# Kernel optimization log

Measured on AMD Instinct MI355X. Metric: run time of the kernel, lower is better.

## Reference

```python
import jax, jax.numpy as jnp
import numpy as np

P = 4096        # n_particles
D = 64          # embedding_dim
H = 4           # attention heads
HD = D // H     # head dim
N = 1_000_000   # n_collisions


def setup_inputs() -> dict:
    key = jax.random.key(0)
    ks = jax.random.split(key, 24)
    s = lambda k, shape, fan: jax.random.normal(k, shape, jnp.float32) / np.sqrt(fan)
    inp = {
        'times': jax.random.normal(ks[0], (N,), jnp.float32),
        'momentum_transfers': jax.random.normal(ks[1], (N,), jnp.float32),
        'positions': jax.random.normal(ks[2], (N,), jnp.float32),
        'particle_pairs': jax.random.randint(ks[3], (N, 2), 0, P),
        # event encoder: Linear(3, D)
        'W_enc': s(ks[4], (3, D), 3), 'b_enc': jnp.zeros((D,), jnp.float32),
        # learned particle embeddings
        'pemb': s(ks[5], (P, D), D),
        # MultiheadAttention projections (math layout: y = x @ W + b)
        'Wq': s(ks[6], (D, D), D), 'bq': jnp.zeros((D,), jnp.float32),
        'Wk': s(ks[7], (D, D), D), 'bk': jnp.zeros((D,), jnp.float32),
        'Wv': s(ks[8], (D, D), D), 'bv': jnp.zeros((D,), jnp.float32),
        'Wo': s(ks[9], (D, D), D), 'bo': jnp.zeros((D,), jnp.float32),
        # mass head: Linear(D, D//2) -> ReLU -> Linear(D//2, 1) -> Softplus
        'Wm1': s(ks[10], (D, D // 2), D), 'bm1': jnp.zeros((D // 2,), jnp.float32),
        'Wm2': s(ks[11], (D // 2, 1), D // 2), 'bm2': jnp.zeros((1,), jnp.float32),
        # diameter head
        'Wd1': s(ks[12], (D, D // 2), D), 'bd1': jnp.zeros((D // 2,), jnp.float32),
        'Wd2': s(ks[13], (D // 2, 1), D // 2), 'bd2': jnp.zeros((1,), jnp.float32),
    }
    return inp


def _forward(times, momentum_transfers, positions, particle_pairs,
             W_enc, b_enc, pemb, Wq, bq, Wk, bk, Wv, bv, Wo, bo,
             Wm1, bm1, Wm2, bm2, Wd1, bd1, Wd2, bd2):
    # 1. embed collision events: (N,3) -> (N,D), tanh
    feats = jnp.stack([times, momentum_transfers, positions], axis=-1)
    emb = jnp.tanh(feats @ W_enc + b_enc)  # (N, D)

    # 2. segment-mean pooling into particle bins (both endpoints of each pair)
    idx = particle_pairs.reshape(-1)                     # (2N,)
    vals = jnp.repeat(emb, 2, axis=0)                    # (2N, D) [p1,p2 per event]
    updates = jax.ops.segment_sum(vals, idx, num_segments=P)          # (P, D)
    counts = jax.ops.segment_sum(jnp.ones_like(idx, jnp.float32), idx,
                                 num_segments=P)                      # (P,)
    counts = jnp.clip(counts, 1.0)
    x = pemb + updates / counts[:, None]                 # (P, D)

    # 3. self-attention over particles (batch of 1)
    q = (x @ Wq + bq).reshape(P, H, HD)
    k = (x @ Wk + bk).reshape(P, H, HD)
    v = (x @ Wv + bv).reshape(P, H, HD)
    scale = 1.0 / np.sqrt(HD)
    scores = jnp.einsum('phd,qhd->hpq', q * scale, k)    # (H, P, P)
    attn = jax.nn.softmax(scores, axis=-1)
    ctx = jnp.einsum('hpq,qhd->phd', attn, v).reshape(P, D)
    x = ctx @ Wo + bo                                    # (P, D)

    # 4. prediction heads
    masses = jax.nn.softplus(
        (jax.nn.relu(x @ Wm1 + bm1) @ Wm2 + bm2)).squeeze(-1)  # (P,)
    diameters = jax.nn.softplus(
        (jax.nn.relu(x @ Wd1 + bd1) @ Wd2 + bd2)).squeeze(-1)  # (P,)
    return masses, diameters


def reference(times, momentum_transfers, positions, particle_pairs,
              W_enc, b_enc, pemb, Wq, bq, Wk, bk, Wv, bv, Wo, bo,
              Wm1, bm1, Wm2, bm2, Wd1, bd1, Wd2, bd2):
    return _forward(times, momentum_transfers, positions, particle_pairs,
                    W_enc, b_enc, pemb, Wq, bq, Wk, bk, Wv, bv, Wo, bo,
                    Wm1, bm1, Wm2, bm2, Wd1, bd1, Wd2, bd2)
```

## Files before the change

kernel.cpp:

```cpp
#include <hip/hip_runtime.h>
#include <math.h>

#define NP 1000000
#define NE (2 * NP)
#define P 4096
#define D 64
#define H 4
#define HD 16

#define NB 256
#define PBT 1024

#define KC 8

typedef short s4v __attribute__((ext_vector_type(4)));
typedef short s8v __attribute__((ext_vector_type(8)));
typedef float f4v __attribute__((ext_vector_type(4)));

__device__ __forceinline__ float softplus_f(float x) {
    return fmaxf(x, 0.0f) + log1pf(__expf(-fabsf(x)));
}
__device__ __forceinline__ unsigned short f2bf_rne(float f) {
    unsigned int b = __float_as_uint(f);
    b += 0x7fffu + ((b >> 16) & 1u);
    return (unsigned short)(b >> 16);
}

__global__ void __launch_bounds__(PBT) hist_pass(const int* __restrict__ pairs,
                                                 int* __restrict__ hists) {
    __shared__ int lh[P];
    const int tid = threadIdx.x, blk = blockIdx.x;
    for (int i = tid; i < P; i += PBT) lh[i] = 0;
    __syncthreads();
    const int lo = (int)(((long long)blk * NE) / NB);
    const int hi = (int)(((long long)(blk + 1) * NE) / NB);
    for (int i = lo + tid; i < hi; i += PBT) atomicAdd(&lh[pairs[i]], 1);
    __syncthreads();
    for (int i = tid; i < P; i += PBT) hists[blk * P + i] = lh[i];
}

__global__ void scan_cols(int* __restrict__ hists, int* __restrict__ totals) {
    int bin = blockIdx.x * 128 + threadIdx.x;
    int p = 0;
    for (int blk = 0; blk < NB; ++blk) {
        int t = hists[blk * P + bin];
        hists[blk * P + bin] = p;
        p += t;
    }
    totals[bin] = p;
}

__global__ void __launch_bounds__(1024) scan_bins(const int* __restrict__ totals,
                                                  int* __restrict__ bin_start) {
    __shared__ int sdat[1024];
    const int t = threadIdx.x;
    int a[4]; int s = 0;
#pragma unroll
    for (int k2 = 0; k2 < 4; ++k2) { a[k2] = totals[t * 4 + k2]; s += a[k2]; }
    sdat[t] = s;
    __syncthreads();
    for (int off = 1; off < 1024; off <<= 1) {
        int v = (t >= off) ? sdat[t - off] : 0;
        __syncthreads();
        sdat[t] += v;
        __syncthreads();
    }
    int run = sdat[t] - s;
#pragma unroll
    for (int k2 = 0; k2 < 4; ++k2) { bin_start[t * 4 + k2] = run; run += a[k2]; }
    if (t == 1023) bin_start[P] = run;
}

__global__ void __launch_bounds__(PBT) place_pass(
        const int* __restrict__ pairs, const float* __restrict__ times,
        const float* __restrict__ mom, const float* __restrict__ pos,
        const int* __restrict__ hists, const int* __restrict__ bin_start,
        float4* __restrict__ sfeats) {
    __shared__ int lc[P];
    __shared__ int loff[P];
    const int tid = threadIdx.x, blk = blockIdx.x;
    for (int i = tid; i < P; i += PBT) {
        lc[i] = 0;
        loff[i] = bin_start[i] + hists[blk * P + i];
    }
    __syncthreads();
    const int lo = (int)(((long long)blk * NE) / NB);
    const int hi = (int)(((long long)(blk + 1) * NE) / NB);
    for (int i = lo + tid; i < hi; i += PBT) {
        int b = pairs[i];
        int ev = i >> 1;
        int r = atomicAdd(&lc[b], 1);
        float4 f; f.x = times[ev]; f.y = mom[ev]; f.z = pos[ev]; f.w = 0.0f;
        sfeats[loff[b] + r] = f;
    }
}

#define GBODY(fv)                                                              \
    {                                                                          \
        float u0 = fmaf(fv.x, w0a[0], fmaf(fv.y, w1a[0], fmaf(fv.z, w2a[0], ba[0]))); \
        float u1 = fmaf(fv.x, w0a[1], fmaf(fv.y, w1a[1], fmaf(fv.z, w2a[1], ba[1]))); \
        float u2 = fmaf(fv.x, w0a[2], fmaf(fv.y, w1a[2], fmaf(fv.z, w2a[2], ba[2]))); \
        float u3 = fmaf(fv.x, w0a[3], fmaf(fv.y, w1a[3], fmaf(fv.z, w2a[3], ba[3]))); \
        float u4 = fmaf(fv.x, w0b[0], fmaf(fv.y, w1b[0], fmaf(fv.z, w2b[0], bbv[0]))); \
        float u5 = fmaf(fv.x, w0b[1], fmaf(fv.y, w1b[1], fmaf(fv.z, w2b[1], bbv[1]))); \
        float u6 = fmaf(fv.x, w0b[2], fmaf(fv.y, w1b[2], fmaf(fv.z, w2b[2], bbv[2]))); \
        float u7 = fmaf(fv.x, w0b[3], fmaf(fv.y, w1b[3], fmaf(fv.z, w2b[3], bbv[3]))); \
        racc[0] += __builtin_amdgcn_rcpf(__builtin_amdgcn_exp2f(u0) + 1.0f);   \
        racc[1] += __builtin_amdgcn_rcpf(__builtin_amdgcn_exp2f(u1) + 1.0f);   \
        racc[2] += __builtin_amdgcn_rcpf(__builtin_amdgcn_exp2f(u2) + 1.0f);   \
        racc[3] += __builtin_amdgcn_rcpf(__builtin_amdgcn_exp2f(u3) + 1.0f);   \
        racc[4] += __builtin_amdgcn_rcpf(__builtin_amdgcn_exp2f(u4) + 1.0f);   \
        racc[5] += __builtin_amdgcn_rcpf(__builtin_amdgcn_exp2f(u5) + 1.0f);   \
        racc[6] += __builtin_amdgcn_rcpf(__builtin_amdgcn_exp2f(u6) + 1.0f);   \
        racc[7] += __builtin_amdgcn_rcpf(__builtin_amdgcn_exp2f(u7) + 1.0f);   \
    }

__global__ void __launch_bounds__(512) gather_kernel(
        const float4* __restrict__ sfeats, const int* __restrict__ bin_start,
        const float* __restrict__ Wenc, const float* __restrict__ benc,
        const float* __restrict__ pemb, float* __restrict__ x) {
    __shared__ float sred[4][16][68];
    const int tid = threadIdx.x;
    const int wv = tid >> 6, ln = tid & 63;
    const int bi = wv >> 1, hw = wv & 1;
    const int es = ln & 7, dg = ln >> 3;
    const int b = blockIdx.x * 4 + bi;
    const int d0 = dg * 8;
    const float C = 2.8853900817779268f;
    f4v w0a = *(const f4v*)(Wenc + d0);          f4v w0b = *(const f4v*)(Wenc + d0 + 4);
    f4v w1a = *(const f4v*)(Wenc + D + d0);      f4v w1b = *(const f4v*)(Wenc + D + d0 + 4);
    f4v w2a = *(const f4v*)(Wenc + 2 * D + d0);  f4v w2b = *(const f4v*)(Wenc + 2 * D + d0 + 4);
    f4v ba  = *(const f4v*)(benc + d0);          f4v bbv = *(const f4v*)(benc + d0 + 4);
    w0a *= C; w0b *= C; w1a *= C; w1b *= C; w2a *= C; w2b *= C; ba *= C; bbv *= C;

    const int s0 = bin_start[b], s1 = bin_start[b + 1];
    const int cnt = s1 - s0;
    const int half = (cnt + 1) >> 1;
    const int lo = s0 + hw * half;
    const int hi = hw ? s1 : (s0 + half);

    float racc[8];
#pragma unroll
    for (int j = 0; j < 8; ++j) racc[j] = 0.0f;
    int ncnt = 0;
    int base = lo;
    for (; base + 16 <= hi; base += 16) {
        float4 f0 = sfeats[base + es];
        float4 f1 = sfeats[base + 8 + es];
        GBODY(f0);
        GBODY(f1);
        ncnt += 2;
    }
    if (base + 8 <= hi) {
        float4 f0 = sfeats[base + es];
        GBODY(f0);
        ncnt += 1;
        base += 8;
    }
    if (base < hi) {
        const int n = hi - base;
        const bool valid = es < n;
        float4 f = valid ? sfeats[base + es] : make_float4(0.f, 0.f, 0.f, 0.f);
        float save[8];
#pragma unroll
        for (int j = 0; j < 8; ++j) save[j] = racc[j];
        GBODY(f);
        if (!valid) {
#pragma unroll
            for (int j = 0; j < 8; ++j) racc[j] = save[j];
        } else {
            ncnt += 1;
        }
    }
    const float fn = (float)ncnt;
    float* sw = &sred[bi][hw * 8 + es][d0];
#pragma unroll
    for (int j = 0; j < 8; ++j) sw[j] = fmaf(-2.0f, racc[j], fn);
    __syncthreads();
    if (tid < 256) {
        int bin = tid >> 6, dim = tid & 63;
        float s = 0.0f;
#pragma unroll
        for (int e2 = 0; e2 < 16; ++e2) s += sred[bin][e2][dim];
        int gb = blockIdx.x * 4 + bin;
        float c2 = (float)(bin_start[gb + 1] - bin_start[gb]);
        x[gb * D + dim] = pemb[gb * D + dim] + s / fmaxf(c2, 1.0f);
    }
}

__global__ void qkv_kernel(const float* __restrict__ x,
                           const float* __restrict__ Wq, const float* __restrict__ bq,
                           const float* __restrict__ Wk, const float* __restrict__ bk,
                           const float* __restrict__ Wv, const float* __restrict__ bv,
                           unsigned short* __restrict__ Qb, unsigned short* __restrict__ Kb,
                           unsigned short* __restrict__ Vb) {
    __shared__ float xs[4][D];
    const int r0 = blockIdx.x * 4;
    const int tid = threadIdx.x;
    xs[tid >> 6][tid & 63] = x[r0 * D + tid];
    __syncthreads();
    const int row = tid >> 6, col = tid & 63;
    float aq = bq[col], ak = bk[col], av = bv[col];
    for (int d = 0; d < D; ++d) {
        float xv = xs[row][d];
        aq = fmaf(xv, Wq[d * D + col], aq);
        ak = fmaf(xv, Wk[d * D + col], ak);
        av = fmaf(xv, Wv[d * D + col], av);
    }
    const int h = col >> 4, hd = col & 15, gr = r0 + row;
    Qb[((h * P + gr) << 4) + hd] = f2bf_rne(aq * 0.3606737602222409f);
    Kb[((h * P + gr) << 4) + hd] = f2bf_rne(ak);
    Vb[(size_t)(h * 16 + hd) * P + gr] = f2bf_rne(av);
}

__global__ void __launch_bounds__(256) flash_kernel(
        const unsigned short* __restrict__ Qb, const unsigned short* __restrict__ Kb,
        const unsigned short* __restrict__ Vb,
        float* __restrict__ pl, float* __restrict__ pout) {
    const int bid = blockIdx.x;
    const int h  = bid & 3;
    const int qt = (bid >> 2) & 63;
    const int kc = bid >> 8;
    const int tid = threadIdx.x;
    const int wv = tid >> 6, lane = tid & 63;
    const int g = lane >> 4, li = lane & 15;
    const int q0 = qt * 64 + wv * 16;

    s8v qf = {0, 0, 0, 0, 0, 0, 0, 0};
    {
        s4v ql = *(const s4v*)(Qb + ((size_t)(h * P + q0 + li) << 4) + 4 * g);
        qf[0] = ql[0]; qf[1] = ql[1]; qf[2] = ql[2]; qf[3] = ql[3];
    }
    const unsigned short* Kh = Kb + ((size_t)(h * P) << 4);
    const unsigned short* Vrow = Vb + (size_t)(h * 16 + li) * P;

    f4v accA = {0.f, 0.f, 0.f, 0.f};
    f4v accB = {0.f, 0.f, 0.f, 0.f};
    float lA = 0.f, lB = 0.f;
    const int kbeg = kc * (P / KC);
    const int kend = kbeg + P / KC;
#pragma unroll 2
    for (int k0 = kbeg; k0 < kend; k0 += 64) {
        s4v t1 = *(const s4v*)(Kh + ((size_t)(k0 + li) << 4) + 4 * g);
        s4v t2 = *(const s4v*)(Kh + ((size_t)(k0 + 16 + li) << 4) + 4 * g);
        s4v t3 = *(const s4v*)(Kh + ((size_t)(k0 + 32 + li) << 4) + 4 * g);
        s4v t4 = *(const s4v*)(Kh + ((size_t)(k0 + 48 + li) << 4) + 4 * g);
        s4v v1 = *(const s4v*)(Vrow + k0 + 4 * g);
        s4v v2 = *(const s4v*)(Vrow + k0 + 16 + 4 * g);
        s4v v3 = *(const s4v*)(Vrow + k0 + 32 + 4 * g);
        s4v v4 = *(const s4v*)(Vrow + k0 + 48 + 4 * g);
        s8v ka1 = {t1[0], t1[1], t1[2], t1[3], 0, 0, 0, 0};
        s8v ka2 = {t2[0], t2[1], t2[2], t2[3], 0, 0, 0, 0};
        s8v ka3 = {t3[0], t3[1], t3[2], t3[3], 0, 0, 0, 0};
        s8v ka4 = {t4[0], t4[1], t4[2], t4[3], 0, 0, 0, 0};
        f4v z = {0.f, 0.f, 0.f, 0.f};
        f4v c1 = __builtin_amdgcn_mfma_f32_16x16x32_bf16(ka1, qf, z, 0, 0, 0);
        f4v c2 = __builtin_amdgcn_mfma_f32_16x16x32_bf16(ka2, qf, z, 0, 0, 0);
        f4v c3 = __builtin_amdgcn_mfma_f32_16x16x32_bf16(ka3, qf, z, 0, 0, 0);
        f4v c4 = __builtin_amdgcn_mfma_f32_16x16x32_bf16(ka4, qf, z, 0, 0, 0);
        float p0 = __builtin_amdgcn_exp2f(c1[0]), p1 = __builtin_amdgcn_exp2f(c1[1]);
        float p2 = __builtin_amdgcn_exp2f(c1[2]), p3 = __builtin_amdgcn_exp2f(c1[3]);
        float p4 = __builtin_amdgcn_exp2f(c2[0]), p5 = __builtin_amdgcn_exp2f(c2[1]);
        float p6 = __builtin_amdgcn_exp2f(c2[2]), p7 = __builtin_amdgcn_exp2f(c2[3]);
        float p8 = __builtin_amdgcn_exp2f(c3[0]), p9 = __builtin_amdgcn_exp2f(c3[1]);
        float pa = __builtin_amdgcn_exp2f(c3[2]), pb = __builtin_amdgcn_exp2f(c3[3]);
        float pc = __builtin_amdgcn_exp2f(c4[0]), pd = __builtin_amdgcn_exp2f(c4[1]);
        float pe = __builtin_amdgcn_exp2f(c4[2]), pf_ = __builtin_amdgcn_exp2f(c4[3]);
        lA += ((p0 + p1) + (p2 + p3)) + ((p4 + p5) + (p6 + p7));
        lB += ((p8 + p9) + (pa + pb)) + ((pc + pd) + (pe + pf_));
        s8v pf1, pf2;
        pf1[0] = (short)(__float_as_uint(p0) >> 16); pf1[1] = (short)(__float_as_uint(p1) >> 16);
        pf1[2] = (short)(__float_as_uint(p2) >> 16); pf1[3] = (short)(__float_as_uint(p3) >> 16);
        pf1[4] = (short)(__float_as_uint(p4) >> 16); pf1[5] = (short)(__float_as_uint(p5) >> 16);
        pf1[6] = (short)(__float_as_uint(p6) >> 16); pf1[7] = (short)(__float_as_uint(p7) >> 16);
        pf2[0] = (short)(__float_as_uint(p8) >> 16); pf2[1] = (short)(__float_as_uint(p9) >> 16);
        pf2[2] = (short)(__float_as_uint(pa) >> 16); pf2[3] = (short)(__float_as_uint(pb) >> 16);
        pf2[4] = (short)(__float_as_uint(pc) >> 16); pf2[5] = (short)(__float_as_uint(pd) >> 16);
        pf2[6] = (short)(__float_as_uint(pe) >> 16); pf2[7] = (short)(__float_as_uint(pf_) >> 16);
        s8v vf1 = {v1[0], v1[1], v1[2], v1[3], v2[0], v2[1], v2[2], v2[3]};
        s8v vf2 = {v3[0], v3[1], v3[2], v3[3], v4[0], v4[1], v4[2], v4[3]};
        accA = __builtin_amdgcn_mfma_f32_16x16x32_bf16(vf1, pf1, accA, 0, 0, 0);
        accB = __builtin_amdgcn_mfma_f32_16x16x32_bf16(vf2, pf2, accB, 0, 0, 0);
    }
    f4v acc = {accA[0] + accB[0], accA[1] + accB[1], accA[2] + accB[2], accA[3] + accB[3]};
    float l = lA + lB;
    l += __shfl_xor(l, 16, 64);
    l += __shfl_xor(l, 32, 64);
    const int q = q0 + li;
    const size_t gidx = (size_t)(h * P + q) * KC + kc;
    *(f4v*)(pout + gidx * 16 + 4 * g) = acc;
    if (lane < 16) pl[gidx] = l;
}

__global__ void attn_merge_kernel(const float* __restrict__ pl, const float* __restrict__ pout,
                                  float* __restrict__ ctx) {
    int gt = blockIdx.x * 256 + threadIdx.x;
    int d4 = gt & 3;
    int gq = gt >> 2;
    float L = 0.f;
    f4v s = {0.f, 0.f, 0.f, 0.f};
    for (int c = 0; c < KC; ++c) {
        L += pl[(size_t)gq * KC + c];
        f4v t = *(const f4v*)(pout + ((size_t)gq * KC + c) * 16 + 4 * d4);
        s[0] += t[0]; s[1] += t[1]; s[2] += t[2]; s[3] += t[3];
    }
    float inv = 1.0f / L;
    int h = gq >> 12, q = gq & 4095;
    f4v r; r[0] = s[0] * inv; r[1] = s[1] * inv; r[2] = s[2] * inv; r[3] = s[3] * inv;
    *(f4v*)(ctx + (size_t)q * D + h * 16 + 4 * d4) = r;
}

__global__ void heads_kernel(const float* __restrict__ ctx,
                             const float* __restrict__ Wo, const float* __restrict__ bo,
                             const float* __restrict__ Wm1, const float* __restrict__ bm1,
                             const float* __restrict__ Wm2, const float* __restrict__ bm2,
                             const float* __restrict__ Wd1, const float* __restrict__ bd1,
                             const float* __restrict__ Wd2, const float* __restrict__ bd2,
                             float* __restrict__ out) {
    __shared__ float cs[4][D];
    __shared__ float x2[4][D];
    __shared__ float hid[4][D];
    const int r0 = blockIdx.x * 4;
    const int tid = threadIdx.x;
    cs[tid >> 6][tid & 63] = ctx[r0 * D + tid];
    __syncthreads();
    const int row = tid >> 6, col = tid & 63;
    float a = bo[col];
    for (int d = 0; d < D; ++d) a = fmaf(cs[row][d], Wo[d * D + col], a);
    x2[row][col] = a;
    __syncthreads();
    const int hc = col & 31;
    const float* W1 = (col < 32) ? Wm1 : Wd1;
    float hsum = (col < 32) ? bm1[hc] : bd1[hc];
    for (int d = 0; d < D; ++d) hsum = fmaf(x2[row][d], W1[d * 32 + hc], hsum);
    hsum = fmaxf(hsum, 0.0f);
    float w2 = (col < 32) ? Wm2[hc] : Wd2[hc];
    hid[row][col] = hsum * w2;
    __syncthreads();
    if (tid < 8) {
        int rr = tid >> 1, which = tid & 1;
        float s = which ? bd2[0] : bm2[0];
        for (int j2 = 0; j2 < 32; ++j2) s += hid[rr][which * 32 + j2];
        out[which * P + r0 + rr] = softplus_f(s);
    }
}

extern "C" void kernel_launch(void* const* d_in, const int* in_sizes, int n_in,
                              void* d_out, int out_size, void* d_ws, size_t ws_size,
                              hipStream_t stream) {
    const float* times = (const float*)d_in[0];
    const float* mom   = (const float*)d_in[1];
    const float* pos   = (const float*)d_in[2];
    const int*   pairs = (const int*)d_in[3];
    const float* Wenc  = (const float*)d_in[4];
    const float* benc  = (const float*)d_in[5];
    const float* pemb  = (const float*)d_in[6];
    const float* Wq = (const float*)d_in[7];   const float* bq = (const float*)d_in[8];
    const float* Wk = (const float*)d_in[9];   const float* bk = (const float*)d_in[10];
    const float* Wv = (const float*)d_in[11];  const float* bv = (const float*)d_in[12];
    const float* Wo = (const float*)d_in[13];  const float* bo = (const float*)d_in[14];
    const float* Wm1 = (const float*)d_in[15]; const float* bm1 = (const float*)d_in[16];
    const float* Wm2 = (const float*)d_in[17]; const float* bm2 = (const float*)d_in[18];
    const float* Wd1 = (const float*)d_in[19]; const float* bd1 = (const float*)d_in[20];
    const float* Wd2 = (const float*)d_in[21]; const float* bd2 = (const float*)d_in[22];

    char* wsb = (char*)d_ws;
    float4* sfeats  = (float4*)wsb;
    int* hists      = (int*)(wsb + (size_t)NE * 16);
    int* totals     = hists + (size_t)NB * P;
    int* bin_start  = totals + P;
    float* x        = (float*)(bin_start + P + 2);
    unsigned short* Qb = (unsigned short*)(x + P * D);
    unsigned short* Kb = Qb + (size_t)H * P * 16;
    unsigned short* Vb = Kb + (size_t)H * P * 16;
    float* pl       = (float*)(Vb + (size_t)H * P * 16);
    float* ctx      = pl + (size_t)H * P * KC;
    float* pout     = (float*)wsb;
    float* out      = (float*)d_out;

    hist_pass<<<NB, PBT, 0, stream>>>(pairs, hists);
    scan_cols<<<32, 128, 0, stream>>>(hists, totals);
    scan_bins<<<1, 1024, 0, stream>>>(totals, bin_start);
    place_pass<<<NB, PBT, 0, stream>>>(pairs, times, mom, pos, hists, bin_start, sfeats);
    gather_kernel<<<P / 4, 512, 0, stream>>>(sfeats, bin_start, Wenc, benc, pemb, x);
    qkv_kernel<<<P / 4, 256, 0, stream>>>(x, Wq, bq, Wk, bk, Wv, bv, Qb, Kb, Vb);
    flash_kernel<<<H * (P / 64) * KC, 256, 0, stream>>>(Qb, Kb, Vb, pl, pout);
    attn_merge_kernel<<<(H * P * 4) / 256, 256, 0, stream>>>(pl, pout, ctx);
    heads_kernel<<<P / 4, 256, 0, stream>>>(ctx, Wo, bo, Wm1, bm1, Wm2, bm2, Wd1, bd1, Wd2, bd2, out);
}
```

Measured before the change: 144.4 us.

## Parallelize column scan with shared tiles, double sort blocks, batch placement loads

Doubles the number of histogram/placement blocks so more CUs work on the counting sort. Each placement thread now handles at most four elements: it issues all its loads up front, then its shared-memory atomics, then its scattered stores, so memory latency overlaps. The per-column prefix scan over block histograms is rewritten to use 1024-thread blocks that stage 64-row tiles in shared memory. This gives coalesced reads and writes instead of one thread walking each column serially. The cost is a histogram buffer twice as large to write, scan and read back.

```diff
diff --git a/kernel.cpp b/kernel.cpp
--- a/kernel.cpp
+++ b/kernel.cpp
@@ -8,8 +8,9 @@
 #define H 4
 #define HD 16
 
-#define NB 256
+#define NB 512
 #define PBT 1024
+#define SCB 128
 
 #define KC 8
 
@@ -36,18 +37,34 @@
     const int hi = (int)(((long long)(blk + 1) * NE) / NB);
     for (int i = lo + tid; i < hi; i += PBT) atomicAdd(&lh[pairs[i]], 1);
     __syncthreads();
-    for (int i = tid; i < P; i += PBT) hists[blk * P + i] = lh[i];
-}
-
-__global__ void scan_cols(int* __restrict__ hists, int* __restrict__ totals) {
-    int bin = blockIdx.x * 128 + threadIdx.x;
-    int p = 0;
-    for (int blk = 0; blk < NB; ++blk) {
-        int t = hists[blk * P + bin];
-        hists[blk * P + bin] = p;
-        p += t;
-    }
-    totals[bin] = p;
+    for (int i = tid; i < P; i += PBT) hists[(size_t)blk * P + i] = lh[i];
+}
+
+__global__ void __launch_bounds__(1024) scan_cols(int* __restrict__ hists,
+                                                  int* __restrict__ totals) {
+    __shared__ int buf[64][SCB];
+    const int bo = blockIdx.x * SCB;
+    const int t = threadIdx.x;
+    const int col = t & (SCB - 1);
+    const int row = t >> 7;
+    int carry = 0;
+    for (int c = 0; c < NB / 64; ++c) {
+#pragma unroll
+        for (int r8 = 0; r8 < 64; r8 += 8)
+            buf[r8 + row][col] = hists[(size_t)(c * 64 + r8 + row) * P + bo + col];
+        __syncthreads();
+        if (t < SCB) {
+            int cr = carry;
+            for (int r = 0; r < 64; ++r) { int v = buf[r][t]; buf[r][t] = cr; cr += v; }
+            carry = cr;
+        }
+        __syncthreads();
+#pragma unroll
+        for (int r8 = 0; r8 < 64; r8 += 8)
+            hists[(size_t)(c * 64 + r8 + row) * P + bo + col] = buf[r8 + row][col];
+        __syncthreads();
+    }
+    if (t < SCB) totals[bo + t] = carry;
 }
 
 __global__ void __launch_bounds__(1024) scan_bins(const int* __restrict__ totals,
@@ -81,18 +98,28 @@
     const int tid = threadIdx.x, blk = blockIdx.x;
     for (int i = tid; i < P; i += PBT) {
         lc[i] = 0;
-        loff[i] = bin_start[i] + hists[blk * P + i];
+        loff[i] = bin_start[i] + hists[(size_t)blk * P + i];
     }
     __syncthreads();
     const int lo = (int)(((long long)blk * NE) / NB);
     const int hi = (int)(((long long)(blk + 1) * NE) / NB);
-    for (int i = lo + tid; i < hi; i += PBT) {
-        int b = pairs[i];
-        int ev = i >> 1;
-        int r = atomicAdd(&lc[b], 1);
-        float4 f; f.x = times[ev]; f.y = mom[ev]; f.z = pos[ev]; f.w = 0.0f;
-        sfeats[loff[b] + r] = f;
-    }
+    int idx[4]; bool vld[4]; int bb[4]; float4 ff[4];
+#pragma unroll
+    for (int j = 0; j < 4; ++j) {
+        idx[j] = lo + tid + j * PBT;
+        vld[j] = idx[j] < hi;
+        int i2 = vld[j] ? idx[j] : lo;
+        int ev = i2 >> 1;
+        bb[j] = pairs[i2];
+        ff[j].x = times[ev]; ff[j].y = mom[ev]; ff[j].z = pos[ev]; ff[j].w = 0.0f;
+    }
+    int rr[4];
+#pragma unroll
+    for (int j = 0; j < 4; ++j)
+        rr[j] = vld[j] ? atomicAdd(&lc[bb[j]], 1) : 0;
+#pragma unroll
+    for (int j = 0; j < 4; ++j)
+        if (vld[j]) sfeats[(size_t)loff[bb[j]] + rr[j]] = ff[j];
 }
 
 #define GBODY(fv)                                                              \
@@ -379,7 +406,7 @@
     float* out      = (float*)d_out;
 
     hist_pass<<<NB, PBT, 0, stream>>>(pairs, hists);
-    scan_cols<<<32, 128, 0, stream>>>(hists, totals);
+    scan_cols<<<P / SCB, 1024, 0, stream>>>(hists, totals);
     scan_bins<<<1, 1024, 0, stream>>>(totals, bin_start);
     place_pass<<<NB, PBT, 0, stream>>>(pairs, times, mom, pos, hists, bin_start, sfeats);
     gather_kernel<<<P / 4, 512, 0, stream>>>(sfeats, bin_start, Wenc, benc, pemb, x);
```

After: 151.5 us. 4.9% more time.
